# Kernel tuning notes

Measured on AMD Instinct MI355X. Metric: run time of the kernel, lower is better.

The kernel has to match this reference:

```python
import jax, jax.numpy as jnp
import numpy as np

NB, B, L, D, H = 4, 4, 1024, 512, 8
E = D // H  # head dim = 64
SCALE = 1.0 / np.sqrt(E)


def setup_inputs() -> dict:
    key = jax.random.key(0)
    ks = jax.random.split(key, 18)
    w = lambda k, shape: (jax.random.normal(k, shape, dtype=jnp.float32) * 0.02)
    inp = {
        'x': jax.random.normal(ks[0], (NB, B, L, D), dtype=jnp.float32),
        # per-block intra-attention projections, stored [in, out] (x @ W + b)
        'Wq': w(ks[1], (NB, D, D)), 'bq': w(ks[2], (NB, D)),
        'Wk': w(ks[3], (NB, D, D)), 'bk': w(ks[4], (NB, D)),
        'Wv': w(ks[5], (NB, D, D)), 'bv': w(ks[6], (NB, D)),
        'Wo': w(ks[7], (NB, D, D)), 'bo': w(ks[8], (NB, D)),
        # shared inter (router) attention projections
        'iWq': w(ks[9], (D, D)), 'ibq': w(ks[10], (D,)),
        'iWk': w(ks[11], (D, D)), 'ibk': w(ks[12], (D,)),
        'iWv': w(ks[13], (D, D)), 'ibv': w(ks[14], (D,)),
        'iWo': w(ks[15], (D, D)), 'ibo': w(ks[16], (D,)),
    }
    return inp


def _full_attn(q, k, v):
    # q,k,v: [..., S, H, E] with batch dims leading; unmasked FullAttention
    scores = jnp.einsum('...lhe,...she->...hls', q, k) * SCALE
    A = jax.nn.softmax(scores, axis=-1)
    return jnp.einsum('...hls,...shd->...lhd', A, v)


def reference(x, Wq, bq, Wk, bk, Wv, bv, Wo, bo,
              iWq, ibq, iWk, ibk, iWv, ibv, iWo, ibo):
    # ---- intra attention, vectorized over the NB blocks ----
    proj = lambda W, b: (jnp.einsum('nbld,nde->nble', x, W) + b[:, None, None, :])
    q = proj(Wq, bq).reshape(NB, B, L, H, E)
    k = proj(Wk, bk).reshape(NB, B, L, H, E)
    v = proj(Wv, bv).reshape(NB, B, L, H, E)
    o = _full_attn(q, k, v).reshape(NB, B, L, D)
    x_intra = jnp.einsum('nbld,nde->nble', o, Wo) + bo[:, None, None, :]

    # ---- inter attention over router tokens (last token of each block) ----
    routers = jnp.transpose(x_intra[:, :, -1, :], (1, 0, 2))  # [B, NB, D]
    rq = (routers @ iWq + ibq).reshape(B, NB, H, E)
    rk = (routers @ iWk + ibk).reshape(B, NB, H, E)
    rv = (routers @ iWv + ibv).reshape(B, NB, H, E)
    ro = _full_attn(rq, rk, rv).reshape(B, NB, D)
    x_inter = ro @ iWo + ibo  # [B, NB, D]

    # replace each block's last (router) token with its inter-attended version
    x_out = x_intra.at[:, :, -1, :].set(jnp.transpose(x_inter, (1, 0, 2)))
    return x_out  # [NB, B, L, D]
```

## Files before the change

### kernel.cpp

```cpp
#include <hip/hip_runtime.h>
#include <math.h>

#define NBV 4
#define BBV 4
#define LLV 1024
#define DDV 512
#define HHV 8
#define EEV 64

typedef unsigned short u16;
typedef _Float16 half8 __attribute__((ext_vector_type(8)));
typedef float f32x4 __attribute__((ext_vector_type(4)));

#define QSCALE 0.1803368801111243f

__device__ __forceinline__ u16 f2h(float f) {
  union { _Float16 h; u16 u; } v; v.h = (_Float16)f; return v.u;
}
__device__ __forceinline__ unsigned pkrtz(float a, float b) {
  typedef __fp16 fp16x2 __attribute__((ext_vector_type(2)));
  union { fp16x2 h; unsigned u; } c;
  c.h = __builtin_amdgcn_cvt_pkrtz(a, b);
  return c.u;
}
__device__ __forceinline__ void gload16(const void* g, void* l) {
  __builtin_amdgcn_global_load_lds(
      (const __attribute__((address_space(1))) unsigned int*)g,
      (__attribute__((address_space(3))) unsigned int*)l, 16, 0, 0);
}

__global__ __launch_bounds__(256) void convert(
    const float* __restrict__ x,
    const float* __restrict__ Wq, const float* __restrict__ Wk,
    const float* __restrict__ Wv, const float* __restrict__ Wo,
    u16* __restrict__ x_t, u16* __restrict__ wt, u16* __restrict__ wo)
{
  const int bid = blockIdx.x;
  if (bid < 4096) {
    const int t = bid * 256 + threadIdx.x;
    const int lane = t & 63;
    const int f = (t >> 6) & 7;
    const int kt = (t >> 9) & 15;
    const int rt = t >> 13;
    const int r = rt * 128 + f * 16 + (lane & 15);
    const int k0 = kt * 32 + (lane >> 4) * 8;
    const float* s = x + (size_t)r * 512 + k0;
    float4 v0 = *(const float4*)s;
    float4 v1 = *(const float4*)(s + 4);
    float vv[8] = {v0.x, v0.y, v0.z, v0.w, v1.x, v1.y, v1.z, v1.w};
    union { u16 s16[8]; uint4 v; } H;
#pragma unroll
    for (int j = 0; j < 8; ++j) H.s16[j] = f2h(vv[j]);
    *(uint4*)(x_t + (size_t)t * 8) = H.v;
  } else {
    const int qkv = (bid < 5632);
    const int t = (qkv ? (bid - 4096) : (bid - 5632)) * 256 + threadIdx.x;
    const int z = t >> 15;
    const int tl = t & 32767;
    const int lane = tl & 63;
    const int f = (tl >> 6) & 7;
    const int kt = (tl >> 9) & 15;
    const int rt = tl >> 13;
    const float* W;
    u16* dst;
    if (qkv) {
      const int nb = z / 3, p = z - nb * 3;
      W = (p == 0 ? Wq : p == 1 ? Wk : Wv) + (size_t)nb * 262144;
      dst = wt;
    } else {
      W = Wo + (size_t)z * 262144;
      dst = wo;
    }
    const int r = rt * 128 + f * 16 + (lane & 15);
    const int k0 = kt * 32 + (lane >> 4) * 8;
    union { u16 s16[8]; uint4 v; } H;
#pragma unroll
    for (int j = 0; j < 8; ++j) H.s16[j] = f2h(W[(size_t)(k0 + j) * 512 + r]);
    *(uint4*)(dst + (size_t)z * 262144 + (size_t)tl * 8) = H.v;
  }
}

template <int MODE>
__global__ __launch_bounds__(256) void gemm_f16(
    const u16* __restrict__ Aw, const u16* __restrict__ Bx,
    const float* __restrict__ bias0, const float* __restrict__ bias1,
    const float* __restrict__ bias2,
    u16* __restrict__ q_b, u16* __restrict__ k_b, u16* __restrict__ v_t,
    float* __restrict__ Cout)
{
  __shared__ __align__(16) u16 SM[17408];
  u16* As = SM;
  u16* Bs = SM + 8192;

  const int tid = threadIdx.x;
  const int lane = tid & 63, w = tid >> 6;
  const int l15 = lane & 15, l4 = lane >> 4;
  const int bid = blockIdx.x;

  int mt, nt, z;
  if (MODE == 0) {
    const int wgid = (bid & 7) * 192 + (bid >> 3);
    mt = wgid & 3; nt = (wgid >> 2) & 31; z = wgid >> 7;
  } else {
    const int wgid = (bid & 7) * 64 + (bid >> 3);
    mt = wgid & 31; nt = (wgid >> 5) & 3; z = wgid >> 7;
  }

  int nb, p;
  const u16 *A, *B;
  if (MODE == 0) {
    nb = z / 3; p = z - nb * 3;
    A = Aw + (size_t)z * 262144;
    B = Bx + (size_t)nb * 2097152;
  } else {
    nb = z; p = 0;
    A = Aw + (size_t)z * 2097152;
    B = Bx + (size_t)z * 262144;
  }

  const f32x4 z4 = {0.f, 0.f, 0.f, 0.f};
  f32x4 acc[4][4];
#pragma unroll
  for (int i = 0; i < 4; ++i)
#pragma unroll
    for (int j = 0; j < 4; ++j) acc[i][j] = z4;

  for (int kt = 0; kt < 8; ++kt) {
    __syncthreads();
#pragma unroll
    for (int s = 0; s < 2; ++s) {
      const u16* ap = A + ((size_t)((mt * 16 + kt * 2 + s) * 8) + w * 2) * 512 + lane * 8;
      const u16* bp = B + ((size_t)((nt * 16 + kt * 2 + s) * 8) + w * 2) * 512 + lane * 8;
      gload16(ap,       As + (s * 8 + w * 2 + 0) * 512);
      gload16(ap + 512, As + (s * 8 + w * 2 + 1) * 512);
      gload16(bp,       Bs + (s * 8 + w * 2 + 0) * 512);
      gload16(bp + 512, Bs + (s * 8 + w * 2 + 1) * 512);
    }
    __syncthreads();

#pragma unroll
    for (int s = 0; s < 2; ++s) {
      half8 a[4], b[4];
#pragma unroll
      for (int m = 0; m < 4; ++m)
        a[m] = *(const half8*)(As + (s * 8 + (w >> 1) * 4 + m) * 512 + lane * 8);
#pragma unroll
      for (int n = 0; n < 4; ++n)
        b[n] = *(const half8*)(Bs + (s * 8 + (w & 1) * 4 + n) * 512 + lane * 8);
#pragma unroll
      for (int m = 0; m < 4; ++m)
#pragma unroll
        for (int n = 0; n < 4; ++n)
          acc[m][n] = __builtin_amdgcn_mfma_f32_16x16x32_f16(a[m], b[n], acc[m][n], 0, 0, 0);
    }
  }

  if (MODE == 0) {
    const float* bias = (p == 0 ? bias0 : p == 1 ? bias1 : bias2) + nb * 512;
    const int hh = w >> 1;
    __syncthreads();
    if (p < 2) {
      const float scl = (p == 0) ? QSCALE : 1.0f;
#pragma unroll
      for (int mm = 0; mm < 4; ++mm) {
        const int c = mm * 4 + l4;
#pragma unroll
        for (int nn = 0; nn < 4; ++nn) {
          const int tok = (w & 1) * 64 + nn * 16 + l15;
          ushort4 pk;
#pragma unroll
          for (int i = 0; i < 4; ++i) {
            const int mf = mt * 128 + hh * 64 + mm * 16 + l4 * 4 + i;
            ((u16*)&pk)[i] = f2h((acc[mm][nn][i] + bias[mf]) * scl);
          }
          *(ushort4*)((char*)SM + hh * 17408 + tok * 136 +
                      ((c ^ (tok & 15)) * 8)) = pk;
        }
      }
      __syncthreads();
      u16* dst = (p == 0 ? q_b : k_b);
#pragma unroll
      for (int i = 0; i < 16; ++i) {
        const int idx = i * 256 + tid;
        const int h2 = idx >> 11, tok = (idx >> 4) & 127, c = idx & 15;
        ushort4 v = *(const ushort4*)((char*)SM + h2 * 17408 + tok * 136 +
                                      ((c ^ (tok & 15)) * 8));
        const int ltok = nt * 128 + tok;
        const int headf = (nb * 4 + (ltok >> 10)) * 8 + mt * 2 + h2;
        *(ushort4*)(dst + (size_t)headf * 65536 + (ltok & 1023) * 64 + c * 4) = v;
      }
    } else {
#pragma unroll
      for (int mm = 0; mm < 4; ++mm) {
#pragma unroll
        for (int nn = 0; nn < 4; ++nn) {
          const int tok = (w & 1) * 64 + nn * 16 + l15;
#pragma unroll
          for (int r = 0; r < 4; ++r) {
            const int e = mm * 16 + l4 * 4 + r;
            const int mf = mt * 128 + hh * 64 + e;
            *(u16*)((char*)SM + hh * 17408 + e * 264 + tok * 2) =
                f2h(acc[mm][nn][r] + bias[mf]);
          }
        }
      }
      __syncthreads();
#pragma unroll
      for (int i = 0; i < 16; ++i) {
        const int idx = i * 256 + tid;
        const int h2 = idx >> 11, rem = idx & 2047;
        const int e = rem >> 5, s = rem & 31;
        uint2 v = *(const uint2*)((char*)SM + h2 * 17408 + e * 264 + s * 8);
        const int headf = (nb * 4 + (nt >> 3)) * 8 + mt * 2 + h2;
        *(uint2*)(v_t + (size_t)headf * 65536 + e * 1024 +
                  (nt & 7) * 128 + s * 4) = v;
      }
    }
  } else {
#pragma unroll
    for (int mm = 0; mm < 4; ++mm) {
#pragma unroll
      for (int nn = 0; nn < 4; ++nn) {
        const int m0 = mt * 128 + ((w >> 1) * 4 + mm) * 16 + l4 * 4;
        const int n  = nt * 128 + ((w & 1) * 4 + nn) * 16 + l15;
        const float bz = bias0[nb * 512 + n];
#pragma unroll
        for (int r = 0; r < 4; ++r)
          Cout[((size_t)nb * 4096 + m0 + r) * 512 + n] = acc[mm][nn][r] + bz;
      }
    }
  }
}

__global__ __launch_bounds__(512, 4) void attn_mfma(
    const u16* __restrict__ Qb, const u16* __restrict__ Kb,
    const u16* __restrict__ Vt, u16* __restrict__ o_t)
{
  __shared__ __align__(16) u16 SM[34816];
  u16* KL = SM;
  u16* VL = SM + 12288;
  u16* PL = SM + 24576;

  const int tid = threadIdx.x;
  const int lane = tid & 63, w = tid >> 6;
  const int l15 = lane & 15, l4 = lane >> 4;
  const int sb = blockIdx.x;
  const int head = sb & 127;
  const int qt = sb >> 7;
  const size_t hbase = (size_t)head * 65536;
  const int q0 = qt * 256;

  const f32x4 z4 = {0.f, 0.f, 0.f, 0.f};
  const _Float16 one_h = (_Float16)1.0f;
  const half8 ones = {one_h, one_h, one_h, one_h, one_h, one_h, one_h, one_h};
  f32x4 oacc[2][4], ls[2];
#pragma unroll
  for (int qm = 0; qm < 2; ++qm) {
    ls[qm] = z4;
#pragma unroll
    for (int ef = 0; ef < 4; ++ef) oacc[qm][ef] = z4;
  }

  const int rowl = lane >> 3;
  const int colx = ((lane & 7) ^ rowl) * 8;

#define STAGE(buf, kt0)                                                        \
  {                                                                            \
    gload16(Kb + hbase + (size_t)((kt0) + w * 8 + rowl) * 64 + colx,           \
            KL + (buf) * 4096 + w * 512);                                      \
    gload16(Vt + hbase + (size_t)(w * 8 + rowl) * 1024 + (kt0) + colx,         \
            VL + (buf) * 4096 + w * 512);                                      \
  }

  half8 qf[2][2];
#pragma unroll
  for (int qm = 0; qm < 2; ++qm) {
    const u16* qp = Qb + hbase + (size_t)(q0 + w * 32 + qm * 16 + l15) * 64 + l4 * 8;
    qf[qm][0] = *(const half8*)qp;
    qf[qm][1] = *(const half8*)(qp + 32);
  }

  STAGE(0, 0);
  STAGE(1, 64);
  STAGE(2, 128);

  char* Pw = (char*)(PL + w * 1280);

  for (int t = 0; t < 16; ++t) {
    const int cur = t % 3;
    if (t <= 13)      { asm volatile("s_waitcnt vmcnt(4)" ::: "memory"); }
    else if (t == 14) { asm volatile("s_waitcnt vmcnt(2)" ::: "memory"); }
    else              { asm volatile("s_waitcnt vmcnt(0)" ::: "memory"); }
    __builtin_amdgcn_sched_barrier(0);
    __builtin_amdgcn_s_barrier();
    __builtin_amdgcn_sched_barrier(0);

    f32x4 st[2][4];
#pragma unroll
    for (int qm = 0; qm < 2; ++qm)
#pragma unroll
      for (int kf = 0; kf < 4; ++kf) st[qm][kf] = z4;

    __builtin_amdgcn_s_setprio(1);
#pragma unroll
    for (int kf = 0; kf < 4; ++kf) {
      const int key = kf * 16 + l15;
      const int swz = (key & 7) << 4;
#pragma unroll
      for (int eh = 0; eh < 2; ++eh) {
        half8 af = *(const half8*)((char*)(KL + cur * 4096) +
                     ((key * 128 + eh * 64 + l4 * 16) ^ swz));
        st[0][kf] = __builtin_amdgcn_mfma_f32_16x16x32_f16(af, qf[0][eh], st[0][kf], 0, 0, 0);
        st[1][kf] = __builtin_amdgcn_mfma_f32_16x16x32_f16(af, qf[1][eh], st[1][kf], 0, 0, 0);
      }
    }
    __builtin_amdgcn_s_setprio(0);

#pragma unroll
    for (int kh = 0; kh < 2; ++kh) {
#pragma unroll
      for (int qm = 0; qm < 2; ++qm) {
        const int row = qm * 16 + l15;
#pragma unroll
        for (int kf2 = 0; kf2 < 2; ++kf2) {
          const int kf = kh * 2 + kf2;
          float e0 = __builtin_amdgcn_exp2f(st[qm][kf][0]);
          float e1 = __builtin_amdgcn_exp2f(st[qm][kf][1]);
          float e2 = __builtin_amdgcn_exp2f(st[qm][kf][2]);
          float e3 = __builtin_amdgcn_exp2f(st[qm][kf][3]);
          uint2 d;
          d.x = pkrtz(e0, e1);
          d.y = pkrtz(e2, e3);
          *(uint2*)(Pw + row * 80 + kf2 * 32 + l4 * 8) = d;
        }
      }
      __builtin_amdgcn_s_setprio(1);
      half8 pa0 = *(const half8*)(Pw + l15 * 80 + l4 * 16);
      half8 pa1 = *(const half8*)(Pw + (16 + l15) * 80 + l4 * 16);
      ls[0] = __builtin_amdgcn_mfma_f32_16x16x32_f16(pa0, ones, ls[0], 0, 0, 0);
      ls[1] = __builtin_amdgcn_mfma_f32_16x16x32_f16(pa1, ones, ls[1], 0, 0, 0);
#pragma unroll
      for (int ef = 0; ef < 4; ++ef) {
        const int e = ef * 16 + l15;
        half8 vb2 = *(const half8*)((char*)(VL + cur * 4096) +
                      ((e * 128 + kh * 64 + l4 * 16) ^ ((e & 7) << 4)));
        oacc[0][ef] = __builtin_amdgcn_mfma_f32_16x16x32_f16(pa0, vb2, oacc[0][ef], 0, 0, 0);
        oacc[1][ef] = __builtin_amdgcn_mfma_f32_16x16x32_f16(pa1, vb2, oacc[1][ef], 0, 0, 0);
      }
      __builtin_amdgcn_s_setprio(0);
    }

    asm volatile("s_waitcnt lgkmcnt(0)" ::: "memory");
    __builtin_amdgcn_sched_barrier(0);
    __builtin_amdgcn_s_barrier();
    __builtin_amdgcn_sched_barrier(0);
    if (t < 13) STAGE(cur, (t + 3) * 64);
  }
#undef STAGE

  char* Ot = (char*)SM;
#pragma unroll
  for (int qm = 0; qm < 2; ++qm) {
    f32x4 iv;
#pragma unroll
    for (int r = 0; r < 4; ++r) iv[r] = 1.0f / ls[qm][r];
#pragma unroll
    for (int ef = 0; ef < 4; ++ef)
#pragma unroll
      for (int r = 0; r < 4; ++r) {
        const int tokl = w * 32 + qm * 16 + l4 * 4 + r;
        const int dl = ef * 16 + l15;
        *(u16*)(Ot + ((tokl * 128 + dl * 2) ^ ((tokl & 7) << 4))) =
            f2h(oacc[qm][ef][r] * iv[r]);
      }
  }
  __syncthreads();

  const int nb = head >> 5, bb = (head >> 3) & 3, h = head & 7;
  u16* abase = o_t + (size_t)nb * 2097152;
#pragma unroll
  for (int i = 0; i < 4; ++i) {
    const int gidx = i * 512 + tid;
    const int rt_loc = gidx >> 10;
    const int rem = gidx & 1023;
    const int kh = rem >> 9, f = (rem >> 6) & 7, ln = rem & 63;
    const int tokl = rt_loc * 128 + f * 16 + (ln & 15);
    const int dl = kh * 32 + (ln >> 4) * 8;
    uint4 vvv = *(const uint4*)(Ot + ((tokl * 128 + dl * 2) ^ ((tokl & 7) << 4)));
    const int rt = bb * 8 + qt * 2 + rt_loc;
    *(uint4*)(abase + ((size_t)((rt * 16 + h * 2 + kh) * 8 + f) * 512 + ln * 8)) = vvv;
  }
}

__global__ __launch_bounds__(256) void inter_qkv(
    const float* __restrict__ xout,
    const float* __restrict__ iWq, const float* __restrict__ iWk, const float* __restrict__ iWv,
    const float* __restrict__ ibq, const float* __restrict__ ibk, const float* __restrict__ ibv,
    float* __restrict__ rq, float* __restrict__ rk, float* __restrict__ rv)
{
    __shared__ float Rs[16][512];
    __shared__ float P[16][68];
    const int tid = threadIdx.x;
    for (int t = tid; t < 2048; t += 256) {
        const int row = t >> 7, k4 = (t & 127) * 4;
        const int n = row & 3, b = row >> 2;
        *(float4*)&Rs[row][k4] =
            *(const float4*)&xout[(((size_t)(n * BBV + b) * LLV) + (LLV - 1)) * DDV + k4];
    }
    __syncthreads();

    const int which = blockIdx.y;
    const float* W    = which == 0 ? iWq : which == 1 ? iWk : iWv;
    const float* bias = which == 0 ? ibq : which == 1 ? ibk : ibv;
    float*       out  = which == 0 ? rq  : which == 1 ? rk  : rv;

    const int cb = blockIdx.x * 64;
    const int c4 = (tid & 15) * 4;
    const int kq = tid >> 4;

    f32x4 acc[16];
#pragma unroll
    for (int r = 0; r < 16; ++r) acc[r] = (f32x4){0.f, 0.f, 0.f, 0.f};

    for (int i = 0; i < 32; ++i) {
        const int k = i * 16 + kq;
        const float4 wv = *(const float4*)&W[(size_t)k * 512 + cb + c4];
#pragma unroll
        for (int r = 0; r < 16; ++r) {
            const float rv_ = Rs[r][k];
            acc[r][0] += rv_ * wv.x;
            acc[r][1] += rv_ * wv.y;
            acc[r][2] += rv_ * wv.z;
            acc[r][3] += rv_ * wv.w;
        }
    }

#pragma unroll
    for (int r = 0; r < 16; ++r) {
        *(f32x4*)&P[kq][c4] = acc[r];
        __syncthreads();
        if (tid < 64) {
            float s = 0.f;
#pragma unroll
            for (int q = 0; q < 16; ++q) s += P[q][tid];
            out[(size_t)r * 512 + cb + tid] = s + bias[cb + tid];
        }
        __syncthreads();
    }
}

__global__ __launch_bounds__(64) void inter_attn(
    const float* __restrict__ rq, const float* __restrict__ rk,
    const float* __restrict__ rv, float* __restrict__ ro)
{
    const int b = blockIdx.x >> 3, h = blockIdx.x & 7;
    const int e = threadIdx.x;
    float qv[4], kv[4], vv[4];
#pragma unroll
    for (int n = 0; n < 4; ++n) {
        const size_t base = (size_t)(b * 4 + n) * 512 + h * 64 + e;
        qv[n] = rq[base]; kv[n] = rk[base]; vv[n] = rv[base];
    }
    float s[4][4];
#pragma unroll
    for (int n = 0; n < 4; ++n)
#pragma unroll
        for (int m = 0; m < 4; ++m) {
            float prod = qv[n] * kv[m];
#pragma unroll
            for (int off = 1; off < 64; off <<= 1) prod += __shfl_xor(prod, off);
            s[n][m] = prod * 0.125f;
        }
#pragma unroll
    for (int n = 0; n < 4; ++n) {
        float mx = fmaxf(fmaxf(s[n][0], s[n][1]), fmaxf(s[n][2], s[n][3]));
        float pr[4], den = 0.f, ov = 0.f;
#pragma unroll
        for (int m = 0; m < 4; ++m) { pr[m] = __expf(s[n][m] - mx); den += pr[m]; }
#pragma unroll
        for (int m = 0; m < 4; ++m) ov += pr[m] * vv[m];
        ro[(size_t)(b * 4 + n) * 512 + h * 64 + e] = ov / den;
    }
}

__global__ __launch_bounds__(256) void inter_out(
    const float* __restrict__ ro, const float* __restrict__ iWo,
    const float* __restrict__ ibo, float* __restrict__ out)
{
    __shared__ float Rs[16][512];
    __shared__ float P[16][68];
    const int tid = threadIdx.x;
    for (int t = tid; t < 2048; t += 256)
        *(float4*)&Rs[t >> 7][(t & 127) * 4] = *(const float4*)&ro[t * 4];
    __syncthreads();

    const int cb = blockIdx.x * 64;
    const int c4 = (tid & 15) * 4;
    const int kq = tid >> 4;

    f32x4 acc[16];
#pragma unroll
    for (int r = 0; r < 16; ++r) acc[r] = (f32x4){0.f, 0.f, 0.f, 0.f};

    for (int i = 0; i < 32; ++i) {
        const int k = i * 16 + kq;
        const float4 wv = *(const float4*)&iWo[(size_t)k * 512 + cb + c4];
#pragma unroll
        for (int r = 0; r < 16; ++r) {
            const float rv_ = Rs[r][k];
            acc[r][0] += rv_ * wv.x;
            acc[r][1] += rv_ * wv.y;
            acc[r][2] += rv_ * wv.z;
            acc[r][3] += rv_ * wv.w;
        }
    }

#pragma unroll
    for (int r = 0; r < 16; ++r) {
        *(f32x4*)&P[kq][c4] = acc[r];
        __syncthreads();
        if (tid < 64) {
            float s = 0.f;
#pragma unroll
            for (int q = 0; q < 16; ++q) s += P[q][tid];
            const int b = r >> 2, n = r & 3;
            out[(((size_t)(n * BBV + b) * LLV) + (LLV - 1)) * DDV + cb + tid] =
                s + ibo[cb + tid];
        }
        __syncthreads();
    }
}

extern "C" void kernel_launch(void* const* d_in, const int* in_sizes, int n_in,
                              void* d_out, int out_size, void* d_ws, size_t ws_size,
                              hipStream_t stream)
{
    (void)in_sizes; (void)n_in; (void)out_size; (void)ws_size;
    const float* x   = (const float*)d_in[0];
    const float* Wq  = (const float*)d_in[1];  const float* bq  = (const float*)d_in[2];
    const float* Wk  = (const float*)d_in[3];  const float* bk  = (const float*)d_in[4];
    const float* Wv  = (const float*)d_in[5];  const float* bv  = (const float*)d_in[6];
    const float* Wo  = (const float*)d_in[7];  const float* bo  = (const float*)d_in[8];
    const float* iWq = (const float*)d_in[9];  const float* ibq = (const float*)d_in[10];
    const float* iWk = (const float*)d_in[11]; const float* ibk = (const float*)d_in[12];
    const float* iWv = (const float*)d_in[13]; const float* ibv = (const float*)d_in[14];
    const float* iWo = (const float*)d_in[15]; const float* ibo = (const float*)d_in[16];
    float* out = (float*)d_out;

    char* W = (char*)d_ws;
    u16* x_t  = (u16*)(W);
    u16* wt   = (u16*)(W + 16777216);
    u16* wo   = (u16*)(W + 33554432);
    u16* q_b  = (u16*)(W + 35651584);
    u16* k_b  = (u16*)(W + 52428800);
    u16* v_t  = (u16*)(W + 69206016);
    u16* o_t  = (u16*)(W + 85983232);
    float* rq = (float*)(W + 102760448);
    float* rk = rq + 8192;
    float* rv = rk + 8192;
    float* ro = rv + 8192;

    convert<<<6144, 256, 0, stream>>>(x, Wq, Wk, Wv, Wo, x_t, wt, wo);
    gemm_f16<0><<<1536, 256, 0, stream>>>(
        wt, x_t, bq, bk, bv, q_b, k_b, v_t, nullptr);
    attn_mfma<<<512, 512, 0, stream>>>(q_b, k_b, v_t, o_t);
    gemm_f16<1><<<512, 256, 0, stream>>>(
        o_t, wo, bo, nullptr, nullptr, nullptr, nullptr, nullptr, out);
    inter_qkv<<<dim3(8, 3), 256, 0, stream>>>(out, iWq, iWk, iWv, ibq, ibk, ibv, rq, rk, rv);
    inter_attn<<<32, 64, 0, stream>>>(rq, rk, rv, ro);
    inter_out<<<8, 256, 0, stream>>>(ro, iWo, ibo, out);
}
```

Before: 145.8 us.

## Triple-buffer GEMM LDS tiles with explicit vmcnt waits and MFMA priority

```diff
diff --git a/kernel.cpp b/kernel.cpp
--- a/kernel.cpp
+++ b/kernel.cpp
@@ -88,9 +88,9 @@
     u16* __restrict__ q_b, u16* __restrict__ k_b, u16* __restrict__ v_t,
     float* __restrict__ Cout)
 {
-  __shared__ __align__(16) u16 SM[17408];
+  __shared__ __align__(16) u16 SM[24576];
   u16* As = SM;
-  u16* Bs = SM + 8192;
+  u16* Bs = SM + 12288;
 
   const int tid = threadIdx.x;
   const int lane = tid & 63, w = tid >> 6;
@@ -125,35 +125,51 @@
 #pragma unroll
     for (int j = 0; j < 4; ++j) acc[i][j] = z4;
 
-  for (int kt = 0; kt < 8; ++kt) {
-    __syncthreads();
-#pragma unroll
-    for (int s = 0; s < 2; ++s) {
-      const u16* ap = A + ((size_t)((mt * 16 + kt * 2 + s) * 8) + w * 2) * 512 + lane * 8;
-      const u16* bp = B + ((size_t)((nt * 16 + kt * 2 + s) * 8) + w * 2) * 512 + lane * 8;
-      gload16(ap,       As + (s * 8 + w * 2 + 0) * 512);
-      gload16(ap + 512, As + (s * 8 + w * 2 + 1) * 512);
-      gload16(bp,       Bs + (s * 8 + w * 2 + 0) * 512);
-      gload16(bp + 512, Bs + (s * 8 + w * 2 + 1) * 512);
-    }
-    __syncthreads();
-
-#pragma unroll
-    for (int s = 0; s < 2; ++s) {
-      half8 a[4], b[4];
-#pragma unroll
-      for (int m = 0; m < 4; ++m)
-        a[m] = *(const half8*)(As + (s * 8 + (w >> 1) * 4 + m) * 512 + lane * 8);
+#define GSTAGE(buf, kt)                                                        \
+  {                                                                            \
+    const u16* ap = A + ((size_t)((mt * 16 + (kt)) * 8) + w * 2) * 512 + lane * 8; \
+    const u16* bp = B + ((size_t)((nt * 16 + (kt)) * 8) + w * 2) * 512 + lane * 8; \
+    gload16(ap,       As + (buf) * 4096 + (w * 2 + 0) * 512);                  \
+    gload16(ap + 512, As + (buf) * 4096 + (w * 2 + 1) * 512);                  \
+    gload16(bp,       Bs + (buf) * 4096 + (w * 2 + 0) * 512);                  \
+    gload16(bp + 512, Bs + (buf) * 4096 + (w * 2 + 1) * 512);                  \
+  }
+
+  GSTAGE(0, 0);
+  GSTAGE(1, 1);
+  GSTAGE(2, 2);
+
+  for (int kt = 0; kt < 16; ++kt) {
+    const int cur = kt % 3;
+    if (kt <= 13)      { asm volatile("s_waitcnt vmcnt(8)" ::: "memory"); }
+    else if (kt == 14) { asm volatile("s_waitcnt vmcnt(4)" ::: "memory"); }
+    else               { asm volatile("s_waitcnt vmcnt(0)" ::: "memory"); }
+    __builtin_amdgcn_sched_barrier(0);
+    __builtin_amdgcn_s_barrier();
+    __builtin_amdgcn_sched_barrier(0);
+
+    half8 a[4], b[4];
+#pragma unroll
+    for (int m = 0; m < 4; ++m)
+      a[m] = *(const half8*)(As + cur * 4096 + ((w >> 1) * 4 + m) * 512 + lane * 8);
+#pragma unroll
+    for (int n = 0; n < 4; ++n)
+      b[n] = *(const half8*)(Bs + cur * 4096 + ((w & 1) * 4 + n) * 512 + lane * 8);
+    __builtin_amdgcn_s_setprio(1);
+#pragma unroll
+    for (int m = 0; m < 4; ++m)
 #pragma unroll
       for (int n = 0; n < 4; ++n)
-        b[n] = *(const half8*)(Bs + (s * 8 + (w & 1) * 4 + n) * 512 + lane * 8);
-#pragma unroll
-      for (int m = 0; m < 4; ++m)
-#pragma unroll
-        for (int n = 0; n < 4; ++n)
-          acc[m][n] = __builtin_amdgcn_mfma_f32_16x16x32_f16(a[m], b[n], acc[m][n], 0, 0, 0);
-    }
-  }
+        acc[m][n] = __builtin_amdgcn_mfma_f32_16x16x32_f16(a[m], b[n], acc[m][n], 0, 0, 0);
+    __builtin_amdgcn_s_setprio(0);
+
+    asm volatile("s_waitcnt lgkmcnt(0)" ::: "memory");
+    __builtin_amdgcn_sched_barrier(0);
+    __builtin_amdgcn_s_barrier();
+    __builtin_amdgcn_sched_barrier(0);
+    if (kt < 13) GSTAGE(cur, kt + 3);
+  }
+#undef GSTAGE
 
   if (MODE == 0) {
     const float* bias = (p == 0 ? bias0 : p == 1 ? bias1 : bias2) + nb * 512;
```

Measured after the change: 146.1 us. Within noise of the previous version (+0.2%).
